# Kernel tuning notes

Measured on AMD Instinct MI355X. Metric: run time of the kernel, lower is better.

Reference implementation:

```python
import jax, jax.numpy as jnp
import numpy as np

FEAT_STRIDE = 16
NMS_THRESH = 0.7
N_PRE = 6000    # eval-mode n_test_pre_nms
N_POST = 300    # eval-mode n_test_post_nms
MIN_SIZE = 16.0
NEG = -1e9
N_ANCHOR = 9


def generate_anchor_base():
    base = 16.0
    ratios = np.array([0.5, 1.0, 2.0], dtype=np.float64)
    scales = np.array([8.0, 16.0, 32.0], dtype=np.float64)
    h = (base * scales[None, :] * np.sqrt(ratios[:, None])).reshape(-1)
    w = (base * scales[None, :] * np.sqrt(1.0 / ratios[:, None])).reshape(-1)
    yc = xc = base / 2.0
    ab = np.stack([yc - h / 2, xc - w / 2, yc + h / 2, xc + w / 2], axis=1)
    return ab.astype(np.float32)  # [9,4] (y1,x1,y2,x2)


def enumerate_anchors(hh, ww):
    ab = generate_anchor_base()                       # [A,4]
    sy = np.arange(hh) * FEAT_STRIDE
    sx = np.arange(ww) * FEAT_STRIDE
    sx, sy = np.meshgrid(sx, sy)
    shift = np.stack([sy.ravel(), sx.ravel(), sy.ravel(), sx.ravel()], axis=1)  # [K,4]
    anchor = (shift[:, None, :] + ab[None, :, :]).reshape(-1, 4)                # [K*A,4]
    return jnp.asarray(anchor.astype(np.float32))


def conv2d(x, w, b, pad):
    y = jax.lax.conv_general_dilated(
        x, w, window_strides=(1, 1), padding=[(pad, pad), (pad, pad)],
        dimension_numbers=('NCHW', 'OIHW', 'NCHW'))
    return y + b[None, :, None, None]


def loc2bbox(anchor, loc):
    # anchor, loc: [K,4]; boxes as (y1,x1,y2,x2), deltas as (dy,dx,dh,dw)
    h = anchor[:, 2] - anchor[:, 0]
    w = anchor[:, 3] - anchor[:, 1]
    yc = anchor[:, 0] + 0.5 * h
    xc = anchor[:, 1] + 0.5 * w
    cy = loc[:, 0] * h + yc
    cx = loc[:, 1] * w + xc
    nh = jnp.exp(loc[:, 2]) * h
    nw = jnp.exp(loc[:, 3]) * w
    return jnp.stack([cy - 0.5 * nh, cx - 0.5 * nw, cy + 0.5 * nh, cx + 0.5 * nw], axis=1)


def iou_matrix(b):
    # b: [N,4] -> [N,N] pairwise IoU (same convention as torchvision.ops.nms)
    area = (b[:, 2] - b[:, 0]) * (b[:, 3] - b[:, 1])
    tl = jnp.maximum(b[:, None, :2], b[None, :, :2])
    br = jnp.minimum(b[:, None, 2:], b[None, :, 2:])
    wh = jnp.clip(br - tl, 0.0)
    inter = wh[..., 0] * wh[..., 1]
    return inter / (area[:, None] + area[None, :] - inter + 1e-9)


def propose(loc, score, anchor, img_h, img_w):
    # loc: [K,4] float, score: [K] fg prob, anchor: [K,4]
    roi = loc2bbox(anchor, loc)
    roi = jnp.stack([
        jnp.clip(roi[:, 0], 0.0, img_h), jnp.clip(roi[:, 1], 0.0, img_w),
        jnp.clip(roi[:, 2], 0.0, img_h), jnp.clip(roi[:, 3], 0.0, img_w)], axis=1)
    hs = roi[:, 2] - roi[:, 0]
    ws = roi[:, 3] - roi[:, 1]
    valid = (hs >= MIN_SIZE) & (ws >= MIN_SIZE)
    score = jnp.where(valid, score, NEG)        # filter-by-size via score masking
    vals, idx = jax.lax.top_k(score, N_PRE)      # descending score sort + pre-NMS cut
    boxes = roi[idx]                             # [N_PRE,4]
    iou = iou_matrix(boxes)
    supp0 = vals <= NEG / 2                      # filtered boxes start suppressed
    ar = jnp.arange(N_PRE)

    def body(i, supp):
        row = (iou[i] > NMS_THRESH) & (ar > i)
        return jnp.where(supp[i], supp, supp | row)

    supp = jax.lax.fori_loop(0, N_PRE, body, supp0)
    keep = ~supp
    kept = jnp.nonzero(keep, size=N_POST, fill_value=0)[0]
    n_keep = jnp.sum(keep)
    valid_out = jnp.arange(N_POST) < n_keep
    rois = jnp.where(valid_out[:, None], boxes[kept], 0.0)  # zero-padded [N_POST,4]
    return rois


def rpn_forward(x, conv1_w, conv1_b, score_w, score_b, loc_w, loc_b, img_h, img_w):
    n, _, hh, ww = x.shape
    anchor = enumerate_anchors(hh, ww)                        # [K*A,4]
    hidden = jax.nn.relu(conv2d(x, conv1_w, conv1_b, 1))      # [n,512,hh,ww]
    rpn_locs = conv2d(hidden, loc_w, loc_b, 0)                # [n,36,hh,ww]
    rpn_locs = rpn_locs.transpose(0, 2, 3, 1).reshape(n, -1, 4)
    raw = conv2d(hidden, score_w, score_b, 0).transpose(0, 2, 3, 1)  # [n,hh,ww,18]
    sm = jax.nn.softmax(raw.reshape(n, hh, ww, N_ANCHOR, 2), axis=4)
    fg = sm[..., 1].reshape(n, -1)                            # [n, K*A]
    rpn_scores = raw.reshape(n, -1, 2)
    rois = jax.vmap(lambda l, s: propose(l, s, anchor, float(img_h), float(img_w)))(rpn_locs, fg)
    roi_indices = jnp.repeat(jnp.arange(n, dtype=jnp.int32), N_POST)
    return rpn_locs, rpn_scores, rois.reshape(-1, 4), roi_indices, anchor


def setup_inputs() -> dict:
    key = jax.random.key(0)
    ks = jax.random.split(key, 7)
    n, c, hh, ww = 2, 512, 50, 84
    mid = 512
    x = jax.random.normal(ks[0], (n, c, hh, ww), dtype=jnp.float32)
    conv1_w = 0.01 * jax.random.normal(ks[1], (mid, c, 3, 3), dtype=jnp.float32)
    conv1_b = jnp.zeros((mid,), dtype=jnp.float32)
    score_w = 0.01 * jax.random.normal(ks[2], (N_ANCHOR * 2, mid, 1, 1), dtype=jnp.float32)
    score_b = jnp.zeros((N_ANCHOR * 2,), dtype=jnp.float32)
    loc_w = 0.01 * jax.random.normal(ks[3], (N_ANCHOR * 4, mid, 1, 1), dtype=jnp.float32)
    loc_b = jnp.zeros((N_ANCHOR * 4,), dtype=jnp.float32)
    return {"x": x, "conv1_w": conv1_w, "conv1_b": conv1_b,
            "score_w": score_w, "score_b": score_b,
            "loc_w": loc_w, "loc_b": loc_b,
            "img_h": 800, "img_w": 1344}


def reference(x, conv1_w, conv1_b, score_w, score_b, loc_w, loc_b, img_h, img_w):
    return rpn_forward(x, conv1_w, conv1_b, score_w, score_b, loc_w, loc_b, img_h, img_w)
```

## Files before the change

kernel.cpp:

```cpp
#include <hip/hip_runtime.h>
#include <hip/hip_bf16.h>
#include <math.h>

#define N_BATCH 2
#define HH 50
#define WW 84
#define NPIX (HH*WW)
#define KA (NPIX*9)
#define N_PRE 6000
#define N_POST 300
#define NMS_T 0.7f
#define NEGV (-1e9f)
#define NWORDS 94

#define OFF_LOCS   0
#define OFF_SCORES (N_BATCH*KA*4)
#define OFF_ROIS   (OFF_SCORES + N_BATCH*KA*2)
#define OFF_RIDX   (OFF_ROIS + N_BATCH*N_POST*4)
#define OFF_ANCH   (OFF_RIDX + N_BATCH*N_POST)

#define WS_HID    0ull
#define WS_ROI    17505600ull
#define WS_ITEMS  18715200ull
#define WS_SITEMS 19320000ull
#define WS_SBOX   19416000ull
#define WS_MASK   19608000ull
#define WS_DIAG   28632000ull
#define WS_HIST   28728000ull
#define WS_ZERO   28736192ull
#define WS_PEXT   28824000ull
#define WS_WT     WS_ITEMS
#define PART_BYTES 17203200ull

typedef unsigned long long u64;
typedef unsigned u32;

#define AS1 __attribute__((address_space(1)))
#define AS3 __attribute__((address_space(3)))

__global__ __launch_bounds__(64) void k_init(const float* __restrict__ w,
    float* __restrict__ wT3, u32* __restrict__ hists, float* __restrict__ zbuf) {
  __shared__ float ls[64][19];
  const int t2 = blockIdx.x, ocb = blockIdx.y;
  const int tid = threadIdx.x;
  if (ocb == 8) {
    if (t2 == 0) {
      for (int i = tid; i < 4 * 2 * 256; i += 64) hists[i] = 0;
      if (tid < 64) zbuf[tid] = 0.f;
    }
    return;
  }
#pragma unroll
  for (int j = 0; j < 18; j++) {
    int idx = tid + j * 64;
    int oc = idx / 18, r = idx % 18;
    ls[oc][r] = w[(size_t)(ocb * 64 + oc) * 4608 + t2 * 18 + r];
  }
  __syncthreads();
  float* outp = wT3 + (size_t)(t2 * 8 + ocb) * 1152;
#pragma unroll
  for (int j = 0; j < 18; j++) {
    int idx = tid + j * 64;
    int q = idx / 64, oc = idx % 64;
    int kxky = q >> 1, icl = q & 1;
    int kx = kxky / 3, ky = kxky % 3;
    outp[idx] = ls[oc][icl * 9 + ky * 3 + kx];
  }
}

#define IC_T 2
__global__ __launch_bounds__(64, 2) void k_conv1(const float* __restrict__ x,
    const float* __restrict__ wT3, const float* __restrict__ zsrc,
    float* __restrict__ p0, float* __restrict__ p1,
    float* __restrict__ p2, float* __restrict__ p3,
    int ics_per) {
  const int ocb = blockIdx.x;
  const int row = blockIdx.y;
  const int icq = blockIdx.z >> 1;
  const int n   = blockIdx.z & 1;
  const int tid = threadIdx.x;
  const int g   = tid & 3;
  const int ocl = tid >> 2;
  const int ics0 = icq * ics_per;
  const int tiles = ics_per / IC_T;

  __shared__ __align__(16) float lx[2][IC_T * 3 * 96];
  __shared__ __align__(16) float lw[2][IC_T * 9 * 64];

  const float* xg = x + ((size_t)n * 512 + ics0) * NPIX;

  int goff[9];
#pragma unroll
  for (int j = 0; j < 9; j++) {
    int idx = tid + j * 64;
    int ic = idx / 288; int rem = idx % 288;
    int rr = rem / 96;  int rem2 = rem % 96;
    int g2 = rem2 / 24; int q = rem2 % 24;
    int grow = row - 1 + rr;
    int gcol = g2 * 21 - 1 + q;
    bool v = ((unsigned)grow < 50u) && ((unsigned)gcol < 84u);
    goff[j] = v ? (ic * NPIX + grow * 84 + gcol) : -1;
  }

  float acc[4][21];
#pragma unroll
  for (int i = 0; i < 4; i++)
#pragma unroll
    for (int p = 0; p < 21; p++) acc[i][p] = 0.f;

  const float* wt0 = wT3 + ((size_t)(ics0 >> 1) * 8 + ocb) * 1152 + tid;

#pragma unroll
  for (int j = 0; j < 9; j++) {
    const float* gp = (goff[j] >= 0) ? (xg + goff[j]) : zsrc;
    __builtin_amdgcn_global_load_lds((const AS1 void*)gp,
                                     (AS3 void*)&lx[0][j * 64], 4, 0, 0);
  }
#pragma unroll
  for (int j = 0; j < 18; j++)
    __builtin_amdgcn_global_load_lds((const AS1 void*)(wt0 + j * 64),
                                     (AS3 void*)&lw[0][j * 64], 4, 0, 0);

  for (int t = 0; t < tiles; t++) {
    const int cur = t & 1;
    asm volatile("s_waitcnt vmcnt(0)" ::: "memory");
    if (t + 1 < tiles) {
      const int nxt = cur ^ 1;
      const int xadv = (t + 1) * IC_T * NPIX;
      const float* wtn = wt0 + (size_t)(t + 1) * 9216;
#pragma unroll
      for (int j = 0; j < 9; j++) {
        const float* gp = (goff[j] >= 0) ? (xg + goff[j] + xadv) : zsrc;
        __builtin_amdgcn_global_load_lds((const AS1 void*)gp,
                                         (AS3 void*)&lx[nxt][j * 64], 4, 0, 0);
      }
#pragma unroll
      for (int j = 0; j < 18; j++)
        __builtin_amdgcn_global_load_lds((const AS1 void*)(wtn + j * 64),
                                         (AS3 void*)&lw[nxt][j * 64], 4, 0, 0);
    }

#pragma unroll
    for (int icl = 0; icl < IC_T; icl++) {
#pragma unroll
      for (int ky = 0; ky < 3; ky++) {
        float xv[24];
        const float* lp = &lx[cur][icl * 288 + ky * 96 + g * 24];
#pragma unroll
        for (int v4 = 0; v4 < 6; v4++) {
          float4 f = *(const float4*)&lp[v4 * 4];
          xv[v4 * 4 + 0] = f.x; xv[v4 * 4 + 1] = f.y;
          xv[v4 * 4 + 2] = f.z; xv[v4 * 4 + 3] = f.w;
        }
#pragma unroll
        for (int kx = 0; kx < 3; kx++) {
          float4 wv = *(const float4*)&lw[cur][((kx * 3 + ky) * IC_T + icl) * 64 + ocl * 4];
          float wa[4] = {wv.x, wv.y, wv.z, wv.w};
#pragma unroll
          for (int i = 0; i < 4; i++)
#pragma unroll
            for (int p = 0; p < 21; p++)
              acc[i][p] = fmaf(wa[i], xv[p + kx], acc[i][p]);
        }
      }
    }
  }

  {
    float* hp = (icq == 0) ? p0 : (icq == 1) ? p1 : (icq == 2) ? p2 : p3;
    int oc = ocb * 64 + ocl * 4;
#pragma unroll
    for (int i = 0; i < 4; i++) {
      float* op = &hp[(size_t)(n * 512 + oc + i) * NPIX + row * 84 + g * 21];
#pragma unroll
      for (int p = 0; p < 21; p++) op[p] = acc[i][p];
    }
  }
}

__global__ __launch_bounds__(256) void k_head(
    const float* __restrict__ p0, const float* __restrict__ p1,
    const float* __restrict__ p2, const float* __restrict__ p3, int nsplit,
    const float* __restrict__ bias,
    const float* __restrict__ sw, const float* __restrict__ sb,
    const float* __restrict__ lww, const float* __restrict__ lb,
    const int* __restrict__ ihp, const int* __restrict__ iwp,
    float* __restrict__ out, float4* __restrict__ roi, u64* __restrict__ items) {
  const int tid = threadIdx.x;
  const int q = tid >> 6;
  const int pxl = tid & 63;
  const int P = blockIdx.x * 64 + pxl;
  const bool valid = P < N_BATCH * NPIX;
  const int n = P / NPIX, p = P - n * NPIX;
  const int o0 = q * 14;
  __shared__ float xt[32][64];
  __shared__ float wt[32][56];
  __shared__ float lall[64][57];

  float acc[14];
#pragma unroll
  for (int o = 0; o < 14; o++) acc[o] = 0.f;

  for (int c0 = 0; c0 < 512; c0 += 32) {
#pragma unroll
    for (int j = 0; j < 8; j++) {
      int idx = tid + j * 256;
      int c = idx >> 6, lp = idx & 63;
      int PP = blockIdx.x * 64 + lp;
      float v = 0.f;
      if (PP < N_BATCH * NPIX) {
        int nn = PP / NPIX, pp = PP - nn * NPIX;
        size_t off = (size_t)(nn * 512 + c0 + c) * NPIX + pp;
        v = p0[off];
        if (nsplit > 1) v += p1[off];
        if (nsplit > 2) { v += p2[off]; v += p3[off]; }
        v += bias[c0 + c];
        v = v > 0.f ? v : 0.f;
      }
      xt[c][lp] = v;
    }
    for (int i = tid; i < 32 * 54; i += 256) {
      int c = i / 54, o = i % 54;
      wt[c][o] = (o < 18) ? sw[o * 512 + c0 + c] : lww[(o - 18) * 512 + c0 + c];
    }
    __syncthreads();
#pragma unroll 4
    for (int c = 0; c < 32; c++) {
      float xv = xt[c][pxl];
      const float* wp = &wt[c][o0];
#pragma unroll
      for (int o = 0; o < 14; o++) acc[o] = fmaf(xv, wp[o], acc[o]);
    }
    __syncthreads();
  }

  if (valid) {
#pragma unroll
    for (int j = 0; j < 14; j++) {
      int o = o0 + j;
      if (o < 54) {
        float v = acc[j] + ((o < 18) ? sb[o] : lb[o - 18]);
        lall[pxl][o] = v;
        if (o < 18) out[OFF_SCORES + ((size_t)n * KA + (size_t)p * 9) * 2 + o] = v;
        else        out[OFF_LOCS + ((size_t)n * KA + (size_t)p * 9) * 4 + (o - 18)] = v;
      }
    }
  }
  __syncthreads();

  if (valid && q == 0) {
    const int pi = p / WW, pj = p - pi * WW;
    const float sy = (float)(pi * 16), sx = (float)(pj * 16);
    const float imh = (float)ihp[0], imw = (float)iwp[0];
#pragma unroll
    for (int a = 0; a < 9; a++) {
      int ri = a / 3, si = a % 3;
      double ratio = (ri == 0) ? 0.5 : ((ri == 1) ? 1.0 : 2.0);
      double scale = (si == 0) ? 8.0 : ((si == 1) ? 16.0 : 32.0);
      double hh = 16.0 * scale * sqrt(ratio);
      double ww = 16.0 * scale * sqrt(1.0 / ratio);
      float ay1 = (float)(8.0 - hh * 0.5), ax1 = (float)(8.0 - ww * 0.5);
      float ay2 = (float)(8.0 + hh * 0.5), ax2 = (float)(8.0 + ww * 0.5);
      float4 A = make_float4(sy + ay1, sx + ax1, sy + ay2, sx + ax2);
      int k = p * 9 + a;
      if (n == 0) ((float4*)out)[OFF_ANCH / 4 + k] = A;
      float r0 = lall[pxl][2 * a], r1 = lall[pxl][2 * a + 1];
      float m = fmaxf(r0, r1);
      float e0 = expf(r0 - m), e1 = expf(r1 - m);
      float fgv = e1 / (e0 + e1);
      float Lx = lall[pxl][18 + 4 * a],     Ly = lall[pxl][18 + 4 * a + 1];
      float Lz = lall[pxl][18 + 4 * a + 2], Lw = lall[pxl][18 + 4 * a + 3];
      float h = A.z - A.x, w = A.w - A.y;
      float yc = A.x + 0.5f * h, xc = A.y + 0.5f * w;
      float cy = Lx * h + yc, cx = Ly * w + xc;
      float nh = expf(Lz) * h, nw = expf(Lw) * w;
      float y1 = cy - 0.5f * nh, x1 = cx - 0.5f * nw;
      float y2 = cy + 0.5f * nh, x2 = cx + 0.5f * nw;
      y1 = fminf(fmaxf(y1, 0.f), imh); y2 = fminf(fmaxf(y2, 0.f), imh);
      x1 = fminf(fmaxf(x1, 0.f), imw); x2 = fminf(fmaxf(x2, 0.f), imw);
      bool ok = ((y2 - y1) >= 16.f) && ((x2 - x1) >= 16.f);
      float sc = ok ? fgv : NEGV;
      u32 u = __float_as_uint(sc);
      u32 key = (u & 0x80000000u) ? ~u : (u | 0x80000000u);
      roi[(size_t)n * KA + k] = make_float4(y1, x1, y2, x2);
      items[(size_t)n * KA + k] = ((u64)key << 32) | (u32)(~(u32)k);
    }
  }
}

__global__ __launch_bounds__(256) void k_pass(const u64* __restrict__ items,
    u32* __restrict__ hists, int p) {
  const int bx = blockIdx.x, b = blockIdx.y;
  const int tid = threadIdx.x;
  __shared__ u32 h8[8 * 256];
  __shared__ u32 lhist[256];
  __shared__ u32 shp[2];
  for (int i = tid; i < 2048; i += 256) h8[i] = 0;

  u32 prefix = 0, need = N_PRE;
  for (int q = 0; q < p; q++) {
    __syncthreads();
    for (int i = tid; i < 256; i += 256) lhist[i] = hists[(q * 2 + b) * 256 + i];
    __syncthreads();
    if (tid == 0) {
      u32 nd = need; int chosen = 0;
      for (int bb = 255; bb >= 0; bb--) {
        if (nd <= lhist[bb]) { chosen = bb; break; }
        nd -= lhist[bb];
      }
      shp[0] = (prefix << 8) | (u32)chosen; shp[1] = nd;
    }
    __syncthreads();
    prefix = shp[0]; need = shp[1];
  }
  __syncthreads();

  const u64* it = items + (size_t)b * KA;
  const int s = 3 - p;
  const int slice = tid & 7;
  for (int i = bx * 256 + tid; i < KA; i += 16 * 256) {
    u32 key = (u32)(it[i] >> 32);
    bool match = (p == 0) || ((key >> ((s + 1) * 8)) == prefix);
    if (match) atomicAdd(&h8[slice * 256 + ((key >> (s * 8)) & 255)], 1u);
  }
  __syncthreads();
  if (tid < 256) {
    u32 sum = 0;
#pragma unroll
    for (int k = 0; k < 8; k++) sum += h8[k * 256 + tid];
    if (sum) atomicAdd(&hists[(p * 2 + b) * 256 + tid], sum);
  }
}

__global__ __launch_bounds__(1024) void k_select2(const u64* __restrict__ items,
    const float4* __restrict__ roi, const u32* __restrict__ hists,
    u64* __restrict__ sitems, float4* __restrict__ sbox) {
  const int b = blockIdx.x;
  const int tid = threadIdx.x;
  const int lane = tid & 63;
  const u64* it = items + (size_t)b * KA;
  __shared__ u64 arr[8192];
  __shared__ u32 hist[256];
  __shared__ u32 sh_prefix, sh_need, sh_cnt;
  if (tid == 0) sh_cnt = 0;

  u32 prefix = 0, need = N_PRE;
  for (int q = 0; q < 4; q++) {
    __syncthreads();
    for (int i = tid; i < 256; i += 1024) hist[i] = hists[(q * 2 + b) * 256 + i];
    __syncthreads();
    if (tid == 0) {
      u32 nd = need; int chosen = 0;
      for (int bb = 255; bb >= 0; bb--) {
        if (nd <= hist[bb]) { chosen = bb; break; }
        nd -= hist[bb];
      }
      sh_prefix = (prefix << 8) | (u32)chosen; sh_need = nd;
    }
    __syncthreads();
    prefix = sh_prefix; need = sh_need;
  }
  u32 kth = prefix;
  __syncthreads();

  for (int i0 = 0; i0 < KA; i0 += 1024) {
    int i = i0 + tid;
    u64 v = (i < KA) ? it[i] : 0ull;
    bool sel = (i < KA) && ((u32)(v >> 32) >= kth);
    u64 bal = __ballot(sel);
    u32 cnt = (u32)__popcll(bal);
    u32 base = 0;
    if (lane == 0 && cnt) base = atomicAdd(&sh_cnt, cnt);
    base = (u32)__shfl((int)base, 0, 64);
    if (sel) {
      u32 pos = base + (u32)__popcll(bal & ((1ull << lane) - 1ull));
      if (pos < 8192) arr[pos] = v;
    }
  }
  __syncthreads();
  u32 T = sh_cnt; if (T > 8192) T = 8192;
  for (int i = (int)T + tid; i < 8192; i += 1024) arr[i] = 0ull;

  for (u32 k = 2; k <= 8192; k <<= 1) {
    for (u32 j = k >> 1; j > 0; j >>= 1) {
      __syncthreads();
#pragma unroll 4
      for (u32 m = tid; m < 4096; m += 1024) {
        u32 mm = m & (j - 1);
        u32 i = ((m - mm) << 1) + mm;
        u32 l = i + j;
        u64 a = arr[i], c = arr[l];
        bool dir = ((i & k) == 0);
        if ((a < c) == dir) { arr[i] = c; arr[l] = a; }
      }
    }
  }
  __syncthreads();
  for (int i = tid; i < N_PRE; i += 1024) {
    u64 v = arr[i];
    sitems[(size_t)b * N_PRE + i] = v;
    u32 kk = ~(u32)(v & 0xffffffffull);
    float4 bx = make_float4(0, 0, 0, 0);
    if (kk < KA) bx = roi[(size_t)b * KA + kk];
    sbox[(size_t)b * N_PRE + i] = bx;
  }
}

__global__ __launch_bounds__(64) void k_mask(const float4* __restrict__ sbox,
    u64* __restrict__ mask, u64* __restrict__ diag) {
  const int cb = blockIdx.x, rb = blockIdx.y, b = blockIdx.z;
  if (cb < rb) return;
  const int tid = threadIdx.x;
  __shared__ float4 cbx[64];
  __shared__ float carea[64];
  int col0 = cb * 64;
  int c = col0 + tid;
  float4 v = (c < N_PRE) ? sbox[(size_t)b * N_PRE + c] : make_float4(0, 0, 0, 0);
  cbx[tid] = v;
  carea[tid] = (v.z - v.x) * (v.w - v.y);
  __syncthreads();
  int row = rb * 64 + tid;
  if (row >= N_PRE) return;
  float4 r = sbox[(size_t)b * N_PRE + row];
  float rarea = (r.z - r.x) * (r.w - r.y);
  u64 word = 0ull;
  for (int j = 0; j < 64; j++) {
    int cc = col0 + j;
    if (cc > row && cc < N_PRE) {
      float4 q = cbx[j];
      float ty = fmaxf(r.x, q.x), tx = fmaxf(r.y, q.y);
      float by = fminf(r.z, q.z), bx = fminf(r.w, q.w);
      float ihh = fmaxf(by - ty, 0.f), iww = fmaxf(bx - tx, 0.f);
      float inter = ihh * iww;
      float iou = inter / (rarea + carea[j] - inter + 1e-9f);
      if (iou > NMS_T) word |= (1ull << j);
    }
  }
  mask[((size_t)b * N_PRE + row) * NWORDS + cb] = word;
  if (cb == rb) diag[(size_t)b * N_PRE + row] = word;
}

__global__ __launch_bounds__(64) void k_nms_out(const u64* __restrict__ sitems,
    const float4* __restrict__ sbox, const u64* __restrict__ mask,
    const u64* __restrict__ diag, float* __restrict__ out) {
  const int b = blockIdx.x;
  const int lane = threadIdx.x;
  __shared__ u64 remv[NWORDS];
  __shared__ u64 pre[NWORDS];
  __shared__ u64 dia[N_PRE];
  __shared__ u32 keep[N_POST];
  for (int i = lane; i < NWORDS; i += 64) { remv[i] = 0ull; pre[i] = 0ull; }
  __syncthreads();
  u32 keyneg = ~__float_as_uint(NEGV);
  for (int i = lane; i < N_PRE; i += 64) {
    dia[i] = diag[(size_t)b * N_PRE + i];
    u32 key = (u32)(sitems[(size_t)b * N_PRE + i] >> 32);
    if (key == keyneg || key == 0u)
      atomicOr(&pre[i >> 6], 1ull << (i & 63));
  }
  if (lane == 0) pre[NWORDS - 1] |= ~((1ull << (N_PRE - 64 * (NWORDS - 1))) - 1ull);
  __syncthreads();

  int kc = 0;
  for (int g = 0; g < NWORDS && kc < N_POST; g++) {
    u64 done = 0ull;
    while (kc < N_POST) {
      u64 cur = remv[g] | pre[g] | done;
      if (cur == ~0ull) break;
      int r0 = -1, r1 = -1, r2 = -1, r3 = -1; int m = 1;
      u64 c2 = cur;
      int bit = __ffsll((long long)(~c2)) - 1;
      r0 = g * 64 + bit; c2 |= (1ull << bit) | dia[r0]; done |= 1ull << bit;
      if (c2 != ~0ull && kc + 1 < N_POST) {
        bit = __ffsll((long long)(~c2)) - 1;
        r1 = g * 64 + bit; c2 |= (1ull << bit) | dia[r1]; done |= 1ull << bit; m = 2;
        if (c2 != ~0ull && kc + 2 < N_POST) {
          bit = __ffsll((long long)(~c2)) - 1;
          r2 = g * 64 + bit; c2 |= (1ull << bit) | dia[r2]; done |= 1ull << bit; m = 3;
          if (c2 != ~0ull && kc + 3 < N_POST) {
            bit = __ffsll((long long)(~c2)) - 1;
            r3 = g * 64 + bit; c2 |= (1ull << bit) | dia[r3]; done |= 1ull << bit; m = 4;
          }
        }
      }
      if (lane == 0) {
        keep[kc] = (u32)r0;
        if (m > 1) keep[kc + 1] = (u32)r1;
        if (m > 2) keep[kc + 2] = (u32)r2;
        if (m > 3) keep[kc + 3] = (u32)r3;
      }
      int j = lane >> 4, l16 = lane & 15;
      int rj = (j == 0) ? r0 : (j == 1) ? r1 : (j == 2) ? r2 : r3;
      if (j < m) {
        const u64* mrow = mask + ((size_t)b * N_PRE + rj) * NWORDS;
        for (int cb = g + l16; cb < NWORDS; cb += 16)
          atomicOr(&remv[cb], mrow[cb]);
      }
      kc += m;
      __syncthreads();
    }
  }
  __syncthreads();
  for (int r = lane; r < N_POST; r += 64) {
    float4 bx = make_float4(0, 0, 0, 0);
    if (r < kc) bx = sbox[(size_t)b * N_PRE + keep[r]];
    ((float4*)out)[OFF_ROIS / 4 + (size_t)b * N_POST + r] = bx;
    out[OFF_RIDX + (size_t)b * N_POST + r] = (float)b;
  }
}

extern "C" void kernel_launch(void* const* d_in, const int* in_sizes, int n_in,
                              void* d_out, int out_size, void* d_ws, size_t ws_size,
                              hipStream_t stream) {
  const float* x   = (const float*)d_in[0];
  const float* c1w = (const float*)d_in[1];
  const float* c1b = (const float*)d_in[2];
  const float* sw  = (const float*)d_in[3];
  const float* sb  = (const float*)d_in[4];
  const float* lw  = (const float*)d_in[5];
  const float* lb  = (const float*)d_in[6];
  const int* ih    = (const int*)d_in[7];
  const int* iw    = (const int*)d_in[8];
  float* out = (float*)d_out;
  char* wsb = (char*)d_ws;

  float* hid   = (float*)(wsb + WS_HID);
  float4* roi  = (float4*)(wsb + WS_ROI);
  u64* items   = (u64*)(wsb + WS_ITEMS);
  u64* sitems  = (u64*)(wsb + WS_SITEMS);
  float4* sbox = (float4*)(wsb + WS_SBOX);
  u64* maskp   = (u64*)(wsb + WS_MASK);
  u64* diagp   = (u64*)(wsb + WS_DIAG);
  u32* hists   = (u32*)(wsb + WS_HIST);
  float* zbuf  = (float*)(wsb + WS_ZERO);
  float* wT3   = (float*)(wsb + WS_WT);

  int nsplit = 1;
  if (ws_size >= WS_PEXT + 3 * PART_BYTES) nsplit = 4;
  else if (ws_size >= WS_PEXT + 1 * PART_BYTES) nsplit = 2;
  float* p1 = (nsplit > 1) ? (float*)(wsb + WS_PEXT) : hid;
  float* p2 = (nsplit > 2) ? (float*)(wsb + WS_PEXT + PART_BYTES) : hid;
  float* p3 = (nsplit > 2) ? (float*)(wsb + WS_PEXT + 2 * PART_BYTES) : hid;

  hipLaunchKernelGGL(k_init, dim3(256, 9), dim3(64), 0, stream, c1w, wT3, hists, zbuf);
  hipLaunchKernelGGL(k_conv1, dim3(8, 50, 2 * nsplit), dim3(64), 0, stream,
                     x, wT3, zbuf, hid, p1, p2, p3, 512 / nsplit);
  hipLaunchKernelGGL(k_head, dim3(132), dim3(256), 0, stream,
                     hid, p1, p2, p3, nsplit, c1b, sw, sb, lw, lb, ih, iw,
                     out, roi, items);
  for (int p = 0; p < 4; p++)
    hipLaunchKernelGGL(k_pass, dim3(16, 2), dim3(256), 0, stream, items, hists, p);
  hipLaunchKernelGGL(k_select2, dim3(2), dim3(1024), 0, stream,
                     items, roi, hists, sitems, sbox);
  hipLaunchKernelGGL(k_mask, dim3(NWORDS, NWORDS, 2), dim3(64), 0, stream, sbox, maskp, diagp);
  hipLaunchKernelGGL(k_nms_out, dim3(2), dim3(64), 0, stream, sitems, sbox, maskp, diagp, out);
}
```

Baseline: 1.108 ms.

## Fuse 16-bit key histogram into head kernel and triangular-index NMS mask grid

Builds a 65536-bin histogram of the top 16 key bits with global atomics inside k_head. This replaces the four separate radix k_pass launches, and k_select2 finds the k-th threshold bin with a prefix scan. The k_mask grid now launches only the upper-triangular blocks, mapped through a closed-form row index, so blocks with cb<rb no longer launch and exit. The trade-off is contention on global atomics and a larger bins buffer that must be zeroed in k_init. The select threshold is now only 16-bit resolution, so more candidates may pass the filter, up to the 8192 capacity.

```diff
diff --git a/kernel.cpp b/kernel.cpp
--- a/kernel.cpp
+++ b/kernel.cpp
@@ -26,10 +26,10 @@
 #define WS_SBOX   19416000ull
 #define WS_MASK   19608000ull
 #define WS_DIAG   28632000ull
-#define WS_HIST   28728000ull
-#define WS_ZERO   28736192ull
+#define WS_ZERO   28728000ull
 #define WS_PEXT   28824000ull
 #define WS_WT     WS_ITEMS
+#define WS_BINS   28152384ull
 #define PART_BYTES 17203200ull
 
 typedef unsigned long long u64;
@@ -39,15 +39,15 @@
 #define AS3 __attribute__((address_space(3)))
 
 __global__ __launch_bounds__(64) void k_init(const float* __restrict__ w,
-    float* __restrict__ wT3, u32* __restrict__ hists, float* __restrict__ zbuf) {
+    float* __restrict__ wT3, u32* __restrict__ bins, float* __restrict__ zbuf) {
   __shared__ float ls[64][19];
   const int t2 = blockIdx.x, ocb = blockIdx.y;
   const int tid = threadIdx.x;
   if (ocb == 8) {
-    if (t2 == 0) {
-      for (int i = tid; i < 4 * 2 * 256; i += 64) hists[i] = 0;
-      if (tid < 64) zbuf[tid] = 0.f;
-    }
+    int base = t2 * 64 + tid;
+#pragma unroll
+    for (int k = 0; k < 8; k++) bins[base + k * 16384] = 0u;
+    if (t2 == 0) zbuf[tid] = 0.f;
     return;
   }
 #pragma unroll
@@ -185,7 +185,8 @@
     const float* __restrict__ sw, const float* __restrict__ sb,
     const float* __restrict__ lww, const float* __restrict__ lb,
     const int* __restrict__ ihp, const int* __restrict__ iwp,
-    float* __restrict__ out, float4* __restrict__ roi, u64* __restrict__ items) {
+    float* __restrict__ out, float4* __restrict__ roi, u64* __restrict__ items,
+    u32* __restrict__ bins) {
   const int tid = threadIdx.x;
   const int q = tid >> 6;
   const int pxl = tid & 63;
@@ -252,6 +253,7 @@
     const int pi = p / WW, pj = p - pi * WW;
     const float sy = (float)(pi * 16), sx = (float)(pj * 16);
     const float imh = (float)ihp[0], imw = (float)iwp[0];
+    const u32 neg16 = (~__float_as_uint(NEGV)) >> 16;
 #pragma unroll
     for (int a = 0; a < 9; a++) {
       int ri = a / 3, si = a % 3;
@@ -284,84 +286,64 @@
       u32 key = (u & 0x80000000u) ? ~u : (u | 0x80000000u);
       roi[(size_t)n * KA + k] = make_float4(y1, x1, y2, x2);
       items[(size_t)n * KA + k] = ((u64)key << 32) | (u32)(~(u32)k);
-    }
-  }
-}
-
-__global__ __launch_bounds__(256) void k_pass(const u64* __restrict__ items,
-    u32* __restrict__ hists, int p) {
-  const int bx = blockIdx.x, b = blockIdx.y;
-  const int tid = threadIdx.x;
-  __shared__ u32 h8[8 * 256];
-  __shared__ u32 lhist[256];
-  __shared__ u32 shp[2];
-  for (int i = tid; i < 2048; i += 256) h8[i] = 0;
-
-  u32 prefix = 0, need = N_PRE;
-  for (int q = 0; q < p; q++) {
-    __syncthreads();
-    for (int i = tid; i < 256; i += 256) lhist[i] = hists[(q * 2 + b) * 256 + i];
-    __syncthreads();
-    if (tid == 0) {
-      u32 nd = need; int chosen = 0;
-      for (int bb = 255; bb >= 0; bb--) {
-        if (nd <= lhist[bb]) { chosen = bb; break; }
-        nd -= lhist[bb];
-      }
-      shp[0] = (prefix << 8) | (u32)chosen; shp[1] = nd;
-    }
-    __syncthreads();
-    prefix = shp[0]; need = shp[1];
-  }
-  __syncthreads();
-
-  const u64* it = items + (size_t)b * KA;
-  const int s = 3 - p;
-  const int slice = tid & 7;
-  for (int i = bx * 256 + tid; i < KA; i += 16 * 256) {
-    u32 key = (u32)(it[i] >> 32);
-    bool match = (p == 0) || ((key >> ((s + 1) * 8)) == prefix);
-    if (match) atomicAdd(&h8[slice * 256 + ((key >> (s * 8)) & 255)], 1u);
-  }
-  __syncthreads();
-  if (tid < 256) {
-    u32 sum = 0;
-#pragma unroll
-    for (int k = 0; k < 8; k++) sum += h8[k * 256 + tid];
-    if (sum) atomicAdd(&hists[(p * 2 + b) * 256 + tid], sum);
+      if (ok) {
+        atomicAdd(&bins[(u32)n * 65536u + (key >> 16)], 1u);
+      }
+      u64 bal0 = __ballot(!ok && n == 0);
+      u64 bal1 = __ballot(!ok && n == 1);
+      if (pxl == 0) {
+        u32 c0n = (u32)__popcll(bal0), c1n = (u32)__popcll(bal1);
+        if (c0n) atomicAdd(&bins[neg16], c0n);
+        if (c1n) atomicAdd(&bins[65536u + neg16], c1n);
+      }
+    }
   }
 }
 
 __global__ __launch_bounds__(1024) void k_select2(const u64* __restrict__ items,
-    const float4* __restrict__ roi, const u32* __restrict__ hists,
+    const float4* __restrict__ roi, const u32* __restrict__ bins16,
     u64* __restrict__ sitems, float4* __restrict__ sbox) {
   const int b = blockIdx.x;
   const int tid = threadIdx.x;
   const int lane = tid & 63;
   const u64* it = items + (size_t)b * KA;
   __shared__ u64 arr[8192];
-  __shared__ u32 hist[256];
-  __shared__ u32 sh_prefix, sh_need, sh_cnt;
+  __shared__ u32 psA[1024], psB[1024];
+  __shared__ u32 sh_kth, sh_cnt;
   if (tid == 0) sh_cnt = 0;
-
-  u32 prefix = 0, need = N_PRE;
-  for (int q = 0; q < 4; q++) {
+  const u32* bins = bins16 + (size_t)b * 65536;
+
+  u32 s = 0;
+#pragma unroll 4
+  for (int j = 0; j < 16; j++) {
+    uint4 v = ((const uint4*)bins)[tid * 16 + j];
+    s += v.x + v.y + v.z + v.w;
+  }
+  psA[tid] = s;
+  __syncthreads();
+  u32* src = psA; u32* dst = psB;
+  for (int off = 1; off < 1024; off <<= 1) {
+    u32 v = src[tid] + ((tid + off < 1024) ? src[tid + off] : 0u);
     __syncthreads();
-    for (int i = tid; i < 256; i += 1024) hist[i] = hists[(q * 2 + b) * 256 + i];
+    dst[tid] = v;
     __syncthreads();
-    if (tid == 0) {
-      u32 nd = need; int chosen = 0;
-      for (int bb = 255; bb >= 0; bb--) {
-        if (nd <= hist[bb]) { chosen = bb; break; }
-        nd -= hist[bb];
-      }
-      sh_prefix = (prefix << 8) | (u32)chosen; sh_need = nd;
-    }
-    __syncthreads();
-    prefix = sh_prefix; need = sh_need;
-  }
-  u32 kth = prefix;
-  __syncthreads();
+    u32* tmp = src; src = dst; dst = tmp;
+  }
+  {
+    u32 Sc = src[tid];
+    u32 Sn = (tid == 1023) ? 0u : src[tid + 1];
+    if (Sc >= N_PRE && Sn < N_PRE) {
+      u32 needq = N_PRE - Sn;
+      u32 cum = 0; int jj = 63;
+      for (; jj > 0; jj--) {
+        cum += bins[tid * 64 + jj];
+        if (cum >= needq) break;
+      }
+      sh_kth = ((u32)(tid * 64 + jj)) << 16;
+    }
+  }
+  __syncthreads();
+  u32 kth = sh_kth;
 
   for (int i0 = 0; i0 < KA; i0 += 1024) {
     int i = i0 + tid;
@@ -408,8 +390,12 @@
 
 __global__ __launch_bounds__(64) void k_mask(const float4* __restrict__ sbox,
     u64* __restrict__ mask, u64* __restrict__ diag) {
-  const int cb = blockIdx.x, rb = blockIdx.y, b = blockIdx.z;
-  if (cb < rb) return;
+  const int m = blockIdx.x;
+  const int b = blockIdx.y;
+  int rb = (int)(94.5 - sqrt(94.5 * 94.5 - 2.0 * (double)m));
+  while (94 * rb - rb * (rb - 1) / 2 > m) rb--;
+  while (94 * (rb + 1) - (rb + 1) * rb / 2 <= m) rb++;
+  const int cb = rb + (m - (94 * rb - rb * (rb - 1) / 2));
   const int tid = threadIdx.x;
   __shared__ float4 cbx[64];
   __shared__ float carea[64];
@@ -531,7 +517,7 @@
   float4* sbox = (float4*)(wsb + WS_SBOX);
   u64* maskp   = (u64*)(wsb + WS_MASK);
   u64* diagp   = (u64*)(wsb + WS_DIAG);
-  u32* hists   = (u32*)(wsb + WS_HIST);
+  u32* bins    = (u32*)(wsb + WS_BINS);
   float* zbuf  = (float*)(wsb + WS_ZERO);
   float* wT3   = (float*)(wsb + WS_WT);
 
@@ -542,16 +528,14 @@
   float* p2 = (nsplit > 2) ? (float*)(wsb + WS_PEXT + PART_BYTES) : hid;
   float* p3 = (nsplit > 2) ? (float*)(wsb + WS_PEXT + 2 * PART_BYTES) : hid;
 
-  hipLaunchKernelGGL(k_init, dim3(256, 9), dim3(64), 0, stream, c1w, wT3, hists, zbuf);
+  hipLaunchKernelGGL(k_init, dim3(256, 9), dim3(64), 0, stream, c1w, wT3, bins, zbuf);
   hipLaunchKernelGGL(k_conv1, dim3(8, 50, 2 * nsplit), dim3(64), 0, stream,
                      x, wT3, zbuf, hid, p1, p2, p3, 512 / nsplit);
   hipLaunchKernelGGL(k_head, dim3(132), dim3(256), 0, stream,
                      hid, p1, p2, p3, nsplit, c1b, sw, sb, lw, lb, ih, iw,
-                     out, roi, items);
-  for (int p = 0; p < 4; p++)
-    hipLaunchKernelGGL(k_pass, dim3(16, 2), dim3(256), 0, stream, items, hists, p);
+                     out, roi, items, bins);
   hipLaunchKernelGGL(k_select2, dim3(2), dim3(1024), 0, stream,
-                     items, roi, hists, sitems, sbox);
-  hipLaunchKernelGGL(k_mask, dim3(NWORDS, NWORDS, 2), dim3(64), 0, stream, sbox, maskp, diagp);
+                     items, roi, bins, sitems, sbox);
+  hipLaunchKernelGGL(k_mask, dim3(4465, 2), dim3(64), 0, stream, sbox, maskp, diagp);
   hipLaunchKernelGGL(k_nms_out, dim3(2), dim3(64), 0, stream, sitems, sbox, maskp, diagp, out);
 }
```

After: 1.094 ms. About the same (-1.3%).
